# Kernel tuning notes

Hardware: AMD Instinct MI355X
Metric: run time of the kernel (lower is better)

The kernel has to match this reference:

```python
import jax, jax.numpy as jnp
import numpy as np

EPS = 1e-7
N_CAPS1 = 1152  # 32 maps * 6 * 6
D_CAPS1 = 8
N_CAPS2 = 10
D_CAPS2 = 16


def squash(s, axis=-1):
    sq = jnp.sum(jnp.square(s), axis=axis, keepdims=True)
    return (sq / (1.0 + sq)) * s / jnp.sqrt(sq + EPS)


def conv2d_relu(x, w, b, stride):
    y = jax.lax.conv_general_dilated(
        x, w, window_strides=(stride, stride), padding='VALID',
        dimension_numbers=('NHWC', 'HWIO', 'NHWC'))
    return jax.nn.relu(y + b)


def setup_inputs() -> dict:
    key = jax.random.key(0)
    ks = jax.random.split(key, 10)
    B = 128
    image = jax.random.normal(ks[0], (B, 28, 28, 1), dtype=jnp.float32)
    target = jax.random.randint(ks[1], (B,), 0, N_CAPS2)
    conv1_w = jax.random.normal(ks[2], (9, 9, 1, 256), dtype=jnp.float32) * 0.05
    conv1_b = jnp.zeros((256,), jnp.float32)
    conv2_w = jax.random.normal(ks[3], (9, 9, 256, 256), dtype=jnp.float32) * 0.01
    conv2_b = jnp.zeros((256,), jnp.float32)
    W = jax.random.normal(ks[4], (1, N_CAPS1, N_CAPS2, D_CAPS2, D_CAPS1), dtype=jnp.float32) * 0.1
    d1_w = jax.random.normal(ks[5], (N_CAPS2 * D_CAPS2, 512), dtype=jnp.float32) * 0.05
    d1_b = jnp.zeros((512,), jnp.float32)
    d2_w = jax.random.normal(ks[6], (512, 1024), dtype=jnp.float32) * 0.05
    d2_b = jnp.zeros((1024,), jnp.float32)
    do_w = jax.random.normal(ks[7], (1024, 28 * 28), dtype=jnp.float32) * 0.05
    do_b = jnp.zeros((28 * 28,), jnp.float32)
    return dict(image=image, target=target, conv1_w=conv1_w, conv1_b=conv1_b,
                conv2_w=conv2_w, conv2_b=conv2_b, W=W,
                d1_w=d1_w, d1_b=d1_b, d2_w=d2_w, d2_b=d2_b, do_w=do_w, do_b=do_b)


def reference(image, target, conv1_w, conv1_b, conv2_w, conv2_b, W,
              d1_w, d1_b, d2_w, d2_b, do_w, do_b):
    B = image.shape[0]
    # Convolutional feature extraction: 28x28x1 -> 20x20x256 -> 6x6x256
    x = conv2d_relu(image, conv1_w, conv1_b, 1)
    x = conv2d_relu(x, conv2_w, conv2_b, 2)
    # Primary capsules [B, 1152, 8]
    pc = squash(x.reshape(B, N_CAPS1, D_CAPS1), axis=-1)
    # Prediction vectors u_hat[b,i,j,d] (einsum replaces tile+matmul)
    u_hat = jnp.einsum('ijdk,bik->bijd', W[0], pc)[..., None]  # [B,1152,10,16,1]
    # --- dynamic routing, 2 rounds ---
    raw = jnp.zeros((B, N_CAPS1, N_CAPS2, 1, 1), jnp.float32)
    c1 = jax.nn.softmax(raw, axis=2)
    s1 = jnp.sum(c1 * u_hat, axis=1, keepdims=True)      # [B,1,10,16,1]
    v1 = squash(s1, axis=-2)
    uv1 = jnp.sum(u_hat * v1, axis=-2, keepdims=True)    # agreement [B,1152,10,1,1]
    raw = raw + uv1
    c2 = jax.nn.softmax(raw, axis=2)
    s2 = jnp.sum(c2 * u_hat, axis=1, keepdims=True)
    v2 = squash(s2, axis=-2)                              # [B,1,10,16,1]
    norm_v2 = jnp.sqrt(jnp.sum(jnp.square(v2), axis=-2, keepdims=True) + EPS)  # [B,1,10,1,1]
    y_pred = jnp.squeeze(jnp.argmax(norm_v2, axis=2), axis=(1, 2))             # [B,1]
    # training=True path: reconstruction mask from target labels
    mask = jax.nn.one_hot(target, N_CAPS2, dtype=jnp.float32).reshape(-1, 1, N_CAPS2, 1, 1)
    masked = v2 * mask
    # Decoder
    h = masked.reshape(B, -1, N_CAPS2 * D_CAPS2)  # [B,1,160]
    h = jax.nn.relu(h @ d1_w + d1_b)
    h = jax.nn.relu(h @ d2_w + d2_b)
    dec = jax.nn.sigmoid(h @ do_w + do_b)         # [B,1,784]
    return (norm_v2, y_pred, dec)
```

## Files before the change

kernel.cpp:

```cpp
#include <hip/hip_runtime.h>
#include <hip/hip_bf16.h>

#define EPSQ 1e-7f

#define BSZ 128
#define M2 4608
#define K2 20736
#define KSTEP64 324

#define WS_C1P   0
#define WS_W2TP  13107200
#define WS_CPART 18415616
#define WS_PC    0
#define WS_S12A  1179648
#define WS_H1    13107200
#define WS_H2    13172736

typedef __attribute__((ext_vector_type(8))) short short8;
typedef __attribute__((ext_vector_type(4))) float floatx4;

#define DOT8(W0, W1, P) ((W0).x*(P)[0] + (W0).y*(P)[1] + (W0).z*(P)[2] + (W0).w*(P)[3] + \
                         (W1).x*(P)[4] + (W1).y*(P)[5] + (W1).z*(P)[6] + (W1).w*(P)[7])

__device__ inline ushort bf16_rne(float x) {
    union { float f; unsigned u; } v; v.f = x;
    unsigned r = v.u + 0x7FFFu + ((v.u >> 16) & 1u);
    return (ushort)(r >> 16);
}
__device__ inline float bf16_to_f(ushort h) {
    union { unsigned u; float f; } v; v.u = ((unsigned)h) << 16;
    return v.f;
}

__global__ __launch_bounds__(256) void convprep_kernel(const float* __restrict__ img,
        const float* __restrict__ w1, const float* __restrict__ b1,
        const float* __restrict__ w2,
        ushort* __restrict__ c1p, ushort* __restrict__ w2tp) {
    __shared__ float sm[4160];
    int t = threadIdx.x;
    int bid = blockIdx.x;
    if (bid < 2560) {
        int b = bid / 20, oh = bid % 20;
        if (t < 252) sm[t] = img[b * 784 + oh * 28 + t];
        __syncthreads();
        float acc[20];
#pragma unroll
        for (int ow = 0; ow < 20; ++ow) acc[ow] = 0.f;
        for (int kh = 0; kh < 9; ++kh) {
            float row[28];
#pragma unroll
            for (int c = 0; c < 28; ++c) row[c] = sm[kh * 28 + c];
#pragma unroll
            for (int kw = 0; kw < 9; ++kw) {
                float wv = w1[(kh * 9 + kw) * 256 + t];
#pragma unroll
                for (int ow = 0; ow < 20; ++ow) acc[ow] += row[kw + ow] * wv;
            }
        }
        float bias = b1[t];
        size_t pbase = ((size_t)(b * 20 + oh) * 20) * 512 + (t >> 3) * 16 + (t & 7);
#pragma unroll
        for (int ow = 0; ow < 20; ++ow) {
            float x = fmaxf(acc[ow] + bias, 0.f);
            ushort h = bf16_rne(x);
            size_t a = pbase + (size_t)ow * 512;
            c1p[a] = h;
            c1p[a + 8] = bf16_rne(x - bf16_to_f(h));
        }
    } else {
        int pb = bid - 2560;
        int kt = pb >> 2, nt = pb & 3;
        int tn = t & 63, t4 = t >> 6;
#pragma unroll
        for (int i = 0; i < 16; ++i) {
            int k = i * 4 + t4;
            sm[k * 65 + tn] = w2[(size_t)(kt * 64 + k) * 256 + nt * 64 + tn];
        }
        __syncthreads();
        int tk = t & 63;
#pragma unroll
        for (int i = 0; i < 16; ++i) {
            int n = i * 4 + t4;
            float x = sm[tk * 65 + n];
            ushort h = bf16_rne(x);
            ushort lo = bf16_rne(x - bf16_to_f(h));
            int kg = kt * 64 + tk;
            int khkw = kg >> 8, ic = kg & 255;
            int knew = (((ic >> 6) * 81 + khkw) << 6) + (ic & 63);
            size_t o = (size_t)(nt * 64 + n) * 41472 + (size_t)(knew >> 3) * 16 + (knew & 7);
            w2tp[o] = h; w2tp[o + 8] = lo;
        }
    }
}

#define LDS_AH 0
#define LDS_AL 4096
#define LDS_BH 8192
#define LDS_BL 16384
__global__ __launch_bounds__(256) void conv2_mfma_kernel(
        const ushort* __restrict__ c1p, const ushort* __restrict__ w2tp,
        float* __restrict__ part, int nsteps, int nwg) {
    int bid = blockIdx.x;
    int v = (bid & 7) * (nwg >> 3) + (bid >> 3);
    int mt = v % 72, grp = v / 72;
    int nt = grp & 1, ks = grp >> 1;
    int t = threadIdx.x;
    int m0 = mt * 64, n0 = nt * 128;
    __shared__ __attribute__((aligned(16))) ushort lds[24576];

    int sr = t >> 3, sc = t & 7;
    int mA0 = m0 + sr, mA1 = m0 + sr + 32;
    int b0_ = mA0 / 36, r0_ = mA0 % 36;
    int b1_ = mA1 / 36, r1_ = mA1 % 36;
    int pp0 = (b0_ * 20 + (r0_ / 6) * 2) * 20 + (r0_ % 6) * 2;
    int pp1 = (b1_ * 20 + (r1_ / 6) * 2) * 20 + (r1_ % 6) * 2;
    size_t wbB = (size_t)(n0 + sr) * 41472 + sc * 16;
    int wOff = sr * 64 + ((sc ^ (sr & 7)) * 8);

    int lane = t & 63, wave = t >> 6;
    int l15 = lane & 15, g = lane >> 4;
    int wrb = (wave >> 1) * 32, wcb = (wave & 1) * 64;

    floatx4 acc[2][4];
#pragma unroll
    for (int mi = 0; mi < 2; ++mi)
#pragma unroll
        for (int nj = 0; nj < 4; ++nj) acc[mi][nj] = (floatx4)0.f;

    int st0 = ks * nsteps;
    uint4 A0h, A1h, A0l, A1l, B0h, B1h, B2h, B3h, B0l, B1l, B2l, B3l;
#define LOADG64(ST) { \
        int gst = (ST); \
        int icc = gst / 81, khkw = gst - icc * 81; \
        int kh = khkw / 9, kw = khkw - kh * 9; \
        int ic2 = icc * 128 + sc * 16;                 \
        size_t a0 = (size_t)(pp0 + kh * 20 + kw) * 512 + ic2; \
        size_t a1 = (size_t)(pp1 + kh * 20 + kw) * 512 + ic2; \
        A0h = *(const uint4*)(c1p + a0); \
        A0l = *(const uint4*)(c1p + a0 + 8); \
        A1h = *(const uint4*)(c1p + a1); \
        A1l = *(const uint4*)(c1p + a1 + 8); \
        size_t bo = wbB + (size_t)gst * 128; \
        B0h = *(const uint4*)(w2tp + bo); \
        B0l = *(const uint4*)(w2tp + bo + 8); \
        B1h = *(const uint4*)(w2tp + bo + (size_t)32 * 41472); \
        B1l = *(const uint4*)(w2tp + bo + (size_t)32 * 41472 + 8); \
        B2h = *(const uint4*)(w2tp + bo + (size_t)64 * 41472); \
        B2l = *(const uint4*)(w2tp + bo + (size_t)64 * 41472 + 8); \
        B3h = *(const uint4*)(w2tp + bo + (size_t)96 * 41472); \
        B3l = *(const uint4*)(w2tp + bo + (size_t)96 * 41472 + 8); }

    LOADG64(st0);
    for (int st = 0; st < nsteps; ++st) {
        __syncthreads();
        *(uint4*)&lds[LDS_AH + wOff]        = A0h;
        *(uint4*)&lds[LDS_AH + wOff + 2048] = A1h;
        *(uint4*)&lds[LDS_AL + wOff]        = A0l;
        *(uint4*)&lds[LDS_AL + wOff + 2048] = A1l;
        *(uint4*)&lds[LDS_BH + wOff]        = B0h;
        *(uint4*)&lds[LDS_BH + wOff + 2048] = B1h;
        *(uint4*)&lds[LDS_BH + wOff + 4096] = B2h;
        *(uint4*)&lds[LDS_BH + wOff + 6144] = B3h;
        *(uint4*)&lds[LDS_BL + wOff]        = B0l;
        *(uint4*)&lds[LDS_BL + wOff + 2048] = B1l;
        *(uint4*)&lds[LDS_BL + wOff + 4096] = B2l;
        *(uint4*)&lds[LDS_BL + wOff + 6144] = B3l;
        __syncthreads();
        if (st + 1 < nsteps) LOADG64(st0 + st + 1);

#pragma unroll
        for (int kk = 0; kk < 2; ++kk) {
            int sl = kk * 4 + g;
            short8 ah[2], al[2], bh[4], bl[4];
#pragma unroll
            for (int mi = 0; mi < 2; ++mi) {
                int r = wrb + mi * 16 + l15;
                int ro = r * 64 + ((sl ^ (r & 7)) * 8);
                ah[mi] = *(const short8*)&lds[LDS_AH + ro];
                al[mi] = *(const short8*)&lds[LDS_AL + ro];
            }
#pragma unroll
            for (int nj = 0; nj < 4; ++nj) {
                int c = wcb + nj * 16 + l15;
                int co = c * 64 + ((sl ^ (c & 7)) * 8);
                bh[nj] = *(const short8*)&lds[LDS_BH + co];
                bl[nj] = *(const short8*)&lds[LDS_BL + co];
            }
#pragma unroll
            for (int mi = 0; mi < 2; ++mi)
#pragma unroll
                for (int nj = 0; nj < 4; ++nj) {
                    acc[mi][nj] = __builtin_amdgcn_mfma_f32_16x16x32_bf16(ah[mi], bh[nj], acc[mi][nj], 0, 0, 0);
                    acc[mi][nj] = __builtin_amdgcn_mfma_f32_16x16x32_bf16(ah[mi], bl[nj], acc[mi][nj], 0, 0, 0);
                    acc[mi][nj] = __builtin_amdgcn_mfma_f32_16x16x32_bf16(al[mi], bh[nj], acc[mi][nj], 0, 0, 0);
                }
        }
    }
    __syncthreads();
    float* ldsf = (float*)lds;
#pragma unroll
    for (int mi = 0; mi < 2; ++mi)
#pragma unroll
        for (int nj = 0; nj < 4; ++nj) {
            int col = wcb + nj * 16 + l15;
            int rw = wrb + mi * 16 + (lane >> 4) * 4;
#pragma unroll
            for (int r = 0; r < 4; ++r)
                ldsf[(rw + r) * 132 + col] = acc[mi][nj][r];
        }
    __syncthreads();
    size_t obase = (size_t)ks * M2 * 256;
#pragma unroll
    for (int i = 0; i < 8; ++i) {
        int f = i * 256 + t;
        int row = f >> 5, c4 = f & 31;
        float4 val = *(const float4*)&ldsf[row * 132 + c4 * 4];
        *(float4*)&part[obase + (size_t)(m0 + row) * 256 + n0 + c4 * 4] = val;
    }
}

__global__ __launch_bounds__(256) void squash_pc_kernel(const float* __restrict__ part,
        const float* __restrict__ b2, float* __restrict__ pc,
        float* __restrict__ s12acc, int nsplit) {
    int m = blockIdx.x;
    int n = threadIdx.x;
    if (m < 160) s12acc[m * 256 + n] = 0.f;
    size_t idx = (size_t)m * 256 + n;
    const size_t stride = (size_t)M2 * 256;
    float v = 0.f;
    for (int s = 0; s < nsplit; ++s) v += part[idx + s * stride];
    v = fmaxf(v + b2[n], 0.f);
    float sq = v * v;
    sq += __shfl_xor(sq, 1, 8);
    sq += __shfl_xor(sq, 2, 8);
    sq += __shfl_xor(sq, 4, 8);
    float scale = sq / ((1.f + sq) * sqrtf(sq + EPSQ));
    pc[idx] = v * scale;
}

__global__ __launch_bounds__(192) void s1part_kernel(const float* __restrict__ Wm,
        const float* __restrict__ pc, float* __restrict__ s1acc) {
    int ic = blockIdx.x, bg = blockIdx.y;
    int i0 = ic * 8, b0 = bg * 16;
    int t = threadIdx.x;
    __shared__ float pcl[16][68];
    for (int e = t; e < 1024; e += 192) {
        int bl = e >> 6, off = e & 63;
        pcl[bl][off] = pc[(size_t)(b0 + bl) * 9216 + i0 * 8 + off];
    }
    __syncthreads();
    if (t >= 160) return;
    float4 w[8][2];
#pragma unroll
    for (int ii = 0; ii < 8; ++ii) {
        const float4* wp = (const float4*)&Wm[(size_t)(i0 + ii) * 1280 + t * 8];
        w[ii][0] = wp[0]; w[ii][1] = wp[1];
    }
    for (int bl = 0; bl < 16; ++bl) {
        float s = 0.f;
#pragma unroll
        for (int ii = 0; ii < 8; ++ii) {
            const float* p = &pcl[bl][ii * 8];
            s += DOT8(w[ii][0], w[ii][1], p);
        }
        atomicAdd(&s1acc[(b0 + bl) * 160 + t], s);
    }
}

__global__ __launch_bounds__(192) void c2s2_kernel(const float* __restrict__ Wm,
        const float* __restrict__ pc, const float* __restrict__ s1acc,
        float* __restrict__ s2acc) {
    int ic = blockIdx.x, bg = blockIdx.y;
    int i0 = ic * 8, b0 = bg * 16;
    int t = threadIdx.x;
    __shared__ float pcl[16][68];
    __shared__ float uvl[8][16][10];
    for (int e = t; e < 1024; e += 192) {
        int bl = e >> 6, off = e & 63;
        pcl[bl][off] = pc[(size_t)(b0 + bl) * 9216 + i0 * 8 + off];
    }
    __syncthreads();
    int j = t >> 4;
    float4 w[8][2];
    if (t < 160) {
#pragma unroll
        for (int ii = 0; ii < 8; ++ii) {
            const float4* wp = (const float4*)&Wm[(size_t)(i0 + ii) * 1280 + t * 8];
            w[ii][0] = wp[0]; w[ii][1] = wp[1];
        }
        for (int bl = 0; bl < 16; ++bl) {
            float s1v = s1acc[(b0 + bl) * 160 + t] * 0.1f;
            float q = s1v * s1v;
            q += __shfl_xor(q, 1, 16);
            q += __shfl_xor(q, 2, 16);
            q += __shfl_xor(q, 4, 16);
            q += __shfl_xor(q, 8, 16);
            float vv = s1v * q / ((1.f + q) * sqrtf(q + EPSQ));
#pragma unroll
            for (int ii = 0; ii < 8; ++ii) {
                const float* p = &pcl[bl][ii * 8];
                float u = DOT8(w[ii][0], w[ii][1], p);
                float pr = u * vv;
                pr += __shfl_xor(pr, 1, 16);
                pr += __shfl_xor(pr, 2, 16);
                pr += __shfl_xor(pr, 4, 16);
                pr += __shfl_xor(pr, 8, 16);
                if ((t & 15) == 0) uvl[ii][bl][j] = pr;
            }
        }
    }
    __syncthreads();
    if (t < 128) {
        int ii = t >> 4, bl = t & 15;
        float* uv = uvl[ii][bl];
        float mx = uv[0];
#pragma unroll
        for (int jj = 1; jj < 10; ++jj) mx = fmaxf(mx, uv[jj]);
        float sum = 0.f;
        float ex[10];
#pragma unroll
        for (int jj = 0; jj < 10; ++jj) { ex[jj] = expf(uv[jj] - mx); sum += ex[jj]; }
        float inv = 1.f / sum;
#pragma unroll
        for (int jj = 0; jj < 10; ++jj) uv[jj] = ex[jj] * inv;
    }
    __syncthreads();
    if (t >= 160) return;
    for (int bl = 0; bl < 16; ++bl) {
        float acc = 0.f;
#pragma unroll
        for (int ii = 0; ii < 8; ++ii) {
            const float* p = &pcl[bl][ii * 8];
            float u = DOT8(w[ii][0], w[ii][1], p);
            acc += uvl[ii][bl][j] * u;
        }
        atomicAdd(&s2acc[(b0 + bl) * 160 + t], acc);
    }
}

#define DGRP 4

__global__ __launch_bounds__(256) void fc1_kernel(const float* __restrict__ s2acc,
        const int* __restrict__ target, const float* __restrict__ w,
        const float* __restrict__ bias, float* __restrict__ out,
        float* __restrict__ h1) {
    int nc = blockIdx.x;
    int b0 = blockIdx.y * DGRP;
    int t = threadIdx.x;
    __shared__ float sk[DGRP][160];
    __shared__ float nl[DGRP][10];
    for (int bb = 0; bb < DGRP; ++bb) {
        if (t < 160) {
            int b = b0 + bb;
            float s = s2acc[b * 160 + t];
            float sq = s * s;
            sq += __shfl_xor(sq, 1, 16);
            sq += __shfl_xor(sq, 2, 16);
            sq += __shfl_xor(sq, 4, 16);
            sq += __shfl_xor(sq, 8, 16);
            float v = s * sq / ((1.f + sq) * sqrtf(sq + EPSQ));
            float vsq = v * v;
            vsq += __shfl_xor(vsq, 1, 16);
            vsq += __shfl_xor(vsq, 2, 16);
            vsq += __shfl_xor(vsq, 4, 16);
            vsq += __shfl_xor(vsq, 8, 16);
            float norm = sqrtf(vsq + EPSQ);
            int j = t >> 4;
            sk[bb][t] = (j == target[b]) ? v : 0.f;
            if ((t & 15) == 0) {
                nl[bb][j] = norm;
                if (nc == 0) out[b * 10 + j] = norm;
            }
        }
    }
    __syncthreads();
    if (nc == 0 && t < DGRP) {
        float best = nl[t][0]; int am = 0;
#pragma unroll
        for (int jj = 1; jj < 10; ++jj) if (nl[t][jj] > best) { best = nl[t][jj]; am = jj; }
        out[1280 + b0 + t] = (float)am;
    }
    int n = nc * 256 + t;
    float acc[DGRP];
#pragma unroll
    for (int bb = 0; bb < DGRP; ++bb) acc[bb] = bias[n];
    for (int k = 0; k < 160; ++k) {
        float wv = w[k * 512 + n];
#pragma unroll
        for (int bb = 0; bb < DGRP; ++bb) acc[bb] += sk[bb][k] * wv;
    }
#pragma unroll
    for (int bb = 0; bb < DGRP; ++bb)
        h1[(size_t)(b0 + bb) * 512 + n] = fmaxf(acc[bb], 0.f);
}

__global__ __launch_bounds__(256) void fc2_kernel(const float* __restrict__ h1,
        const float* __restrict__ w, const float* __restrict__ bias,
        float* __restrict__ h2) {
    int nc = blockIdx.x;
    int b0 = blockIdx.y * DGRP;
    int t = threadIdx.x;
    __shared__ float sk[DGRP][512];
    for (int e = t; e < DGRP * 512; e += 256) {
        int bb = e >> 9, k = e & 511;
        sk[bb][k] = h1[(size_t)(b0 + bb) * 512 + k];
    }
    __syncthreads();
    int n = nc * 256 + t;
    float acc[DGRP];
#pragma unroll
    for (int bb = 0; bb < DGRP; ++bb) acc[bb] = bias[n];
    for (int k = 0; k < 512; ++k) {
        float wv = w[(size_t)k * 1024 + n];
#pragma unroll
        for (int bb = 0; bb < DGRP; ++bb) acc[bb] += sk[bb][k] * wv;
    }
#pragma unroll
    for (int bb = 0; bb < DGRP; ++bb)
        h2[(size_t)(b0 + bb) * 1024 + n] = fmaxf(acc[bb], 0.f);
}

__global__ __launch_bounds__(256) void fc3_kernel(const float* __restrict__ h2,
        const float* __restrict__ w, const float* __restrict__ bias,
        float* __restrict__ out) {
    int nc = blockIdx.x;
    int b0 = blockIdx.y * DGRP;
    int t = threadIdx.x;
    __shared__ float sk[DGRP][1024];
    for (int e = t; e < DGRP * 1024; e += 256) {
        int bb = e >> 10, k = e & 1023;
        sk[bb][k] = h2[(size_t)(b0 + bb) * 1024 + k];
    }
    __syncthreads();
    if (t >= 196) return;
    int n = nc * 196 + t;
    float acc[DGRP];
#pragma unroll
    for (int bb = 0; bb < DGRP; ++bb) acc[bb] = bias[n];
    for (int k = 0; k < 1024; ++k) {
        float wv = w[(size_t)k * 784 + n];
#pragma unroll
        for (int bb = 0; bb < DGRP; ++bb) acc[bb] += sk[bb][k] * wv;
    }
#pragma unroll
    for (int bb = 0; bb < DGRP; ++bb)
        out[1408 + (size_t)(b0 + bb) * 784 + n] = 1.f / (1.f + expf(-acc[bb]));
}

extern "C" void kernel_launch(void* const* d_in, const int* in_sizes, int n_in,
                              void* d_out, int out_size, void* d_ws, size_t ws_size,
                              hipStream_t stream) {
    const float* image = (const float*)d_in[0];
    const int*   target = (const int*)d_in[1];
    const float* w1  = (const float*)d_in[2];
    const float* b1  = (const float*)d_in[3];
    const float* w2  = (const float*)d_in[4];
    const float* b2  = (const float*)d_in[5];
    const float* Wm  = (const float*)d_in[6];
    const float* d1w = (const float*)d_in[7];
    const float* d1b = (const float*)d_in[8];
    const float* d2w = (const float*)d_in[9];
    const float* d2b = (const float*)d_in[10];
    const float* dow = (const float*)d_in[11];
    const float* dob = (const float*)d_in[12];
    float* out = (float*)d_out;
    float* ws  = (float*)d_ws;

    ushort* c1p  = (ushort*)(ws + WS_C1P);
    ushort* w2tp = (ushort*)(ws + WS_W2TP);

    int ksplit = 4;
    if (ws_size >= (size_t)(18415616 + 12 * 1179648) * 4) ksplit = 12;
    else if (ws_size >= (size_t)(18415616 + 6 * 1179648) * 4) ksplit = 6;
    int nsteps = KSTEP64 / ksplit;
    int nwg = 144 * ksplit;

    float* s1acc = ws + WS_S12A;
    float* s2acc = ws + WS_S12A + 20480;

    convprep_kernel<<<3856, 256, 0, stream>>>(image, w1, b1, w2, c1p, w2tp);
    conv2_mfma_kernel<<<nwg, 256, 0, stream>>>(c1p, w2tp, ws + WS_CPART, nsteps, nwg);
    squash_pc_kernel<<<4608, 256, 0, stream>>>(ws + WS_CPART, b2, ws + WS_PC,
                                               ws + WS_S12A, ksplit);
    s1part_kernel<<<dim3(144, 8), 192, 0, stream>>>(Wm, ws + WS_PC, s1acc);
    c2s2_kernel<<<dim3(144, 8), 192, 0, stream>>>(Wm, ws + WS_PC, s1acc, s2acc);
    fc1_kernel<<<dim3(2, BSZ / DGRP), 256, 0, stream>>>(s2acc, target, d1w, d1b,
                                                        out, ws + WS_H1);
    fc2_kernel<<<dim3(4, BSZ / DGRP), 256, 0, stream>>>(ws + WS_H1, d2w, d2b, ws + WS_H2);
    fc3_kernel<<<dim3(4, BSZ / DGRP), 256, 0, stream>>>(ws + WS_H2, dow, dob, out);
}
```

Before: 406.4 us.

## Replace split-K partial buffers with atomic accumulation and fuse squash into routing

```diff
diff --git a/kernel.cpp b/kernel.cpp
--- a/kernel.cpp
+++ b/kernel.cpp
@@ -5,16 +5,18 @@
 
 #define BSZ 128
 #define M2 4608
-#define K2 20736
 #define KSTEP64 324
+#define KSPLIT 12
+#define NSTEPS 27
+#define NWG 1728
 
 #define WS_C1P   0
 #define WS_W2TP  13107200
-#define WS_CPART 18415616
-#define WS_PC    0
+#define WS_ACC   18415616
 #define WS_S12A  1179648
 #define WS_H1    13107200
 #define WS_H2    13172736
+#define WS_S12B  19595264
 
 typedef __attribute__((ext_vector_type(8))) short short8;
 typedef __attribute__((ext_vector_type(4))) float floatx4;
@@ -35,10 +37,15 @@
 __global__ __launch_bounds__(256) void convprep_kernel(const float* __restrict__ img,
         const float* __restrict__ w1, const float* __restrict__ b1,
         const float* __restrict__ w2,
-        ushort* __restrict__ c1p, ushort* __restrict__ w2tp) {
+        ushort* __restrict__ c1p, ushort* __restrict__ w2tp,
+        float* __restrict__ accb, float* __restrict__ s12acc) {
     __shared__ float sm[4160];
     int t = threadIdx.x;
     int bid = blockIdx.x;
+    for (size_t z = (size_t)bid * 256 + t; z < 1179648; z += (size_t)3856 * 256)
+        accb[z] = 0.f;
+    if (bid < 160) s12acc[bid * 256 + t] = 0.f;
+
     if (bid < 2560) {
         int b = bid / 20, oh = bid % 20;
         if (t < 252) sm[t] = img[b * 784 + oh * 28 + t];
@@ -99,9 +106,9 @@
 #define LDS_BL 16384
 __global__ __launch_bounds__(256) void conv2_mfma_kernel(
         const ushort* __restrict__ c1p, const ushort* __restrict__ w2tp,
-        float* __restrict__ part, int nsteps, int nwg) {
+        float* __restrict__ accb) {
     int bid = blockIdx.x;
-    int v = (bid & 7) * (nwg >> 3) + (bid >> 3);
+    int v = (bid & 7) * (NWG >> 3) + (bid >> 3);
     int mt = v % 72, grp = v / 72;
     int nt = grp & 1, ks = grp >> 1;
     int t = threadIdx.x;
@@ -127,13 +134,13 @@
 #pragma unroll
         for (int nj = 0; nj < 4; ++nj) acc[mi][nj] = (floatx4)0.f;
 
-    int st0 = ks * nsteps;
+    int st0 = ks * NSTEPS;
     uint4 A0h, A1h, A0l, A1l, B0h, B1h, B2h, B3h, B0l, B1l, B2l, B3l;
 #define LOADG64(ST) { \
         int gst = (ST); \
         int icc = gst / 81, khkw = gst - icc * 81; \
         int kh = khkw / 9, kw = khkw - kh * 9; \
-        int ic2 = icc * 128 + sc * 16;                 \
+        int ic2 = icc * 128 + sc * 16; \
         size_t a0 = (size_t)(pp0 + kh * 20 + kw) * 512 + ic2; \
         size_t a1 = (size_t)(pp1 + kh * 20 + kw) * 512 + ic2; \
         A0h = *(const uint4*)(c1p + a0); \
@@ -151,7 +158,7 @@
         B3l = *(const uint4*)(w2tp + bo + (size_t)96 * 41472 + 8); }
 
     LOADG64(st0);
-    for (int st = 0; st < nsteps; ++st) {
+    for (int st = 0; st < NSTEPS; ++st) {
         __syncthreads();
         *(uint4*)&lds[LDS_AH + wOff]        = A0h;
         *(uint4*)&lds[LDS_AH + wOff + 2048] = A1h;
@@ -166,7 +173,7 @@
         *(uint4*)&lds[LDS_BL + wOff + 4096] = B2l;
         *(uint4*)&lds[LDS_BL + wOff + 6144] = B3l;
         __syncthreads();
-        if (st + 1 < nsteps) LOADG64(st0 + st + 1);
+        if (st + 1 < NSTEPS) LOADG64(st0 + st + 1);
 
 #pragma unroll
         for (int kk = 0; kk < 2; ++kk) {
@@ -209,44 +216,42 @@
                 ldsf[(rw + r) * 132 + col] = acc[mi][nj][r];
         }
     __syncthreads();
-    size_t obase = (size_t)ks * M2 * 256;
 #pragma unroll
     for (int i = 0; i < 8; ++i) {
         int f = i * 256 + t;
         int row = f >> 5, c4 = f & 31;
         float4 val = *(const float4*)&ldsf[row * 132 + c4 * 4];
-        *(float4*)&part[obase + (size_t)(m0 + row) * 256 + n0 + c4 * 4] = val;
-    }
-}
-
-__global__ __launch_bounds__(256) void squash_pc_kernel(const float* __restrict__ part,
-        const float* __restrict__ b2, float* __restrict__ pc,
-        float* __restrict__ s12acc, int nsplit) {
-    int m = blockIdx.x;
-    int n = threadIdx.x;
-    if (m < 160) s12acc[m * 256 + n] = 0.f;
-    size_t idx = (size_t)m * 256 + n;
-    const size_t stride = (size_t)M2 * 256;
-    float v = 0.f;
-    for (int s = 0; s < nsplit; ++s) v += part[idx + s * stride];
-    v = fmaxf(v + b2[n], 0.f);
-    float sq = v * v;
-    sq += __shfl_xor(sq, 1, 8);
-    sq += __shfl_xor(sq, 2, 8);
-    sq += __shfl_xor(sq, 4, 8);
-    float scale = sq / ((1.f + sq) * sqrtf(sq + EPSQ));
-    pc[idx] = v * scale;
+        float* dst = &accb[(size_t)(m0 + row) * 256 + n0 + c4 * 4];
+        atomicAdd(dst + 0, val.x);
+        atomicAdd(dst + 1, val.y);
+        atomicAdd(dst + 2, val.z);
+        atomicAdd(dst + 3, val.w);
+    }
 }
 
 __global__ __launch_bounds__(192) void s1part_kernel(const float* __restrict__ Wm,
-        const float* __restrict__ pc, float* __restrict__ s1acc) {
+        const float* __restrict__ accb, const float* __restrict__ b2,
+        float* __restrict__ s1acc) {
     int ic = blockIdx.x, bg = blockIdx.y;
     int i0 = ic * 8, b0 = bg * 16;
     int t = threadIdx.x;
     __shared__ float pcl[16][68];
     for (int e = t; e < 1024; e += 192) {
         int bl = e >> 6, off = e & 63;
-        pcl[bl][off] = pc[(size_t)(b0 + bl) * 9216 + i0 * 8 + off];
+        int f = i0 * 8 + off;
+        float v = accb[(size_t)(b0 + bl) * 9216 + f] + b2[f & 255];
+        pcl[bl][off] = fmaxf(v, 0.f);
+    }
+    __syncthreads();
+    for (int e = t; e < 128; e += 192) {
+        int bl = e >> 3, gg = e & 7;
+        float* p = &pcl[bl][gg * 8];
+        float sq = 0.f;
+#pragma unroll
+        for (int d = 0; d < 8; ++d) sq += p[d] * p[d];
+        float scale = sq / ((1.f + sq) * sqrtf(sq + EPSQ));
+#pragma unroll
+        for (int d = 0; d < 8; ++d) p[d] *= scale;
     }
     __syncthreads();
     if (t >= 160) return;
@@ -268,8 +273,8 @@
 }
 
 __global__ __launch_bounds__(192) void c2s2_kernel(const float* __restrict__ Wm,
-        const float* __restrict__ pc, const float* __restrict__ s1acc,
-        float* __restrict__ s2acc) {
+        const float* __restrict__ accb, const float* __restrict__ b2,
+        const float* __restrict__ s1acc, float* __restrict__ s2acc) {
     int ic = blockIdx.x, bg = blockIdx.y;
     int i0 = ic * 8, b0 = bg * 16;
     int t = threadIdx.x;
@@ -277,7 +282,20 @@
     __shared__ float uvl[8][16][10];
     for (int e = t; e < 1024; e += 192) {
         int bl = e >> 6, off = e & 63;
-        pcl[bl][off] = pc[(size_t)(b0 + bl) * 9216 + i0 * 8 + off];
+        int f = i0 * 8 + off;
+        float v = accb[(size_t)(b0 + bl) * 9216 + f] + b2[f & 255];
+        pcl[bl][off] = fmaxf(v, 0.f);
+    }
+    __syncthreads();
+    for (int e = t; e < 128; e += 192) {
+        int bl = e >> 3, gg = e & 7;
+        float* p = &pcl[bl][gg * 8];
+        float sq = 0.f;
+#pragma unroll
+        for (int d = 0; d < 8; ++d) sq += p[d] * p[d];
+        float scale = sq / ((1.f + sq) * sqrtf(sq + EPSQ));
+#pragma unroll
+        for (int d = 0; d < 8; ++d) p[d] *= scale;
     }
     __syncthreads();
     int j = t >> 4;
@@ -468,22 +486,15 @@
 
     ushort* c1p  = (ushort*)(ws + WS_C1P);
     ushort* w2tp = (ushort*)(ws + WS_W2TP);
-
-    int ksplit = 4;
-    if (ws_size >= (size_t)(18415616 + 12 * 1179648) * 4) ksplit = 12;
-    else if (ws_size >= (size_t)(18415616 + 6 * 1179648) * 4) ksplit = 6;
-    int nsteps = KSTEP64 / ksplit;
-    int nwg = 144 * ksplit;
-
-    float* s1acc = ws + WS_S12A;
-    float* s2acc = ws + WS_S12A + 20480;
-
-    convprep_kernel<<<3856, 256, 0, stream>>>(image, w1, b1, w2, c1p, w2tp);
-    conv2_mfma_kernel<<<nwg, 256, 0, stream>>>(c1p, w2tp, ws + WS_CPART, nsteps, nwg);
-    squash_pc_kernel<<<4608, 256, 0, stream>>>(ws + WS_CPART, b2, ws + WS_PC,
-                                               ws + WS_S12A, ksplit);
-    s1part_kernel<<<dim3(144, 8), 192, 0, stream>>>(Wm, ws + WS_PC, s1acc);
-    c2s2_kernel<<<dim3(144, 8), 192, 0, stream>>>(Wm, ws + WS_PC, s1acc, s2acc);
+    float* accb  = ws + WS_ACC;
+    float* s1acc = ws + WS_S12B;
+    float* s2acc = ws + WS_S12B + 20480;
+
+    convprep_kernel<<<3856, 256, 0, stream>>>(image, w1, b1, w2, c1p, w2tp,
+                                              accb, s1acc);
+    conv2_mfma_kernel<<<NWG, 256, 0, stream>>>(c1p, w2tp, accb);
+    s1part_kernel<<<dim3(144, 8), 192, 0, stream>>>(Wm, accb, b2, s1acc);
+    c2s2_kernel<<<dim3(144, 8), 192, 0, stream>>>(Wm, accb, b2, s1acc, s2acc);
     fc1_kernel<<<dim3(2, BSZ / DGRP), 256, 0, stream>>>(s2acc, target, d1w, d1b,
                                                         out, ws + WS_H1);
     fc2_kernel<<<dim3(4, BSZ / DGRP), 256, 0, stream>>>(ws + WS_H1, d2w, d2b, ws + WS_H2);
```

Result: slower. 496.4 us (+22.2%).
